# Kernel optimization log

Measured on AMD Instinct MI355X. Metric: run time of the kernel, lower is better.

## Reference

```python
import jax, jax.numpy as jnp
import numpy as np

T_, N_, DIN, D, HEADS, WW, E_, DPE = 8, 20000, 128, 128, 4, 4, 320000, 8
DH = D // HEADS
NEG = -1e30
EPS_GATE = 1e-6


def setup_inputs() -> dict:
    key = jax.random.key(0)
    ks = jax.random.split(key, 10)
    return {
        "H_tilde": jax.random.normal(ks[0], (T_, N_, DIN), jnp.float32),
        "S": jax.random.uniform(ks[1], (T_, N_), jnp.float32),
        "Wq": jax.random.normal(ks[2], (D, DIN), jnp.float32) * 0.05,
        "Wkh": jax.random.normal(ks[3], (D, DIN), jnp.float32) * 0.05,
        "Wkpe": jax.random.normal(ks[4], (D, DPE), jnp.float32) * 0.05,
        "Wv": jax.random.normal(ks[5], (D, DIN), jnp.float32) * 0.05,
        "pe_table": jax.random.normal(ks[6], (WW + 1, DPE), jnp.float32),
        "rel_bias": jax.random.normal(ks[7], (WW + 1,), jnp.float32),
        "src": jax.random.randint(ks[8], (E_,), 0, N_),
        "dst": jax.random.randint(ks[9], (E_,), 0, N_),
    }


def reference(H_tilde, S, Wq, Wkh, Wkpe, Wv, pe_table, rel_bias, src, dst):
    T, N, _ = H_tilde.shape
    H, dh, W = HEADS, DH, WW
    scale = dh ** -0.5
    dtype = H_tilde.dtype

    # Projections (torch Linear: x @ W.T). W_k over concat([H, pe]) splits additively.
    Q = (H_tilde @ Wq.T).reshape(T, N, H, dh)
    K0 = (H_tilde @ Wkh.T).reshape(T, N, H, dh)
    V = (H_tilde @ Wv.T).reshape(T, N, H, dh)
    pe_k = (pe_table @ Wkpe.T).reshape(W + 1, H, dh)
    gate = jnp.log(jnp.clip(S, 0.0, 1.0) + EPS_GATE)  # (T, N)

    # Pad W zero-steps in front so a length-(W+1) slice at t covers t-W..t.
    pad = lambda x: jnp.concatenate([jnp.zeros((W,) + x.shape[1:], x.dtype), x], axis=0)
    Kp, Vp, gp = pad(K0), pad(V), pad(gate)

    def step(_, tq):
        t, Qt = tq  # Qt: (N, H, dh)
        Kwin = jax.lax.dynamic_slice_in_dim(Kp, t, W + 1, 0)[::-1]  # (W+1,N,H,dh), dt=0..W
        Vwin = jax.lax.dynamic_slice_in_dim(Vp, t, W + 1, 0)[::-1]
        gwin = jax.lax.dynamic_slice_in_dim(gp, t, W + 1, 0)[::-1]  # (W+1, N)
        Qd = Qt[dst]  # (E, H, dh)

        scores = []
        for dt in range(W + 1):
            Ks = Kwin[dt][src] + pe_k[dt][None]  # (E, H, dh)
            s = (jnp.einsum('ehc,ehc->eh', Qd, Ks) * scale
                 + rel_bias[dt] + gwin[dt][src][:, None])
            scores.append(jnp.where(dt <= t, s, NEG))  # mask dt > t (W_eff = min(W, t))
        sc = jnp.stack(scores)  # (W+1, E, H)

        # Segment softmax over incoming edges of each dst node, jointly over dt.
        mx = jax.ops.segment_max(sc.transpose(1, 0, 2), dst, num_segments=N)  # (N,W+1,H)
        mx = mx.max(axis=1)  # (N, H)
        valid = (jnp.arange(W + 1) <= t)[:, None, None]
        ex = jnp.where(valid, jnp.exp(sc - mx[dst][None]), 0.0)  # (W+1, E, H)

        denom = jax.ops.segment_sum(ex.sum(axis=0), dst, num_segments=N)  # (N, H)
        numer = jnp.zeros((N, H, dh), dtype)
        for dt in range(W + 1):
            contrib = ex[dt][:, :, None] * Vwin[dt][src]  # (E, H, dh)
            numer = numer + jax.ops.segment_sum(contrib, dst, num_segments=N)

        msg = numer / jnp.maximum(denom, 1e-12)[:, :, None]  # (N, H, dh)
        return None, msg.reshape(N, H * dh)

    _, M_out = jax.lax.scan(step, None, (jnp.arange(T), Q))
    return M_out  # (T, N, d)
```

## Files before the change

kernel.cpp:

```cpp
#include <hip/hip_runtime.h>

typedef unsigned short u16;
typedef unsigned int u32;
typedef __attribute__((ext_vector_type(8))) __bf16 bf16x8;
typedef __attribute__((ext_vector_type(4))) float f32x4;
typedef __attribute__((ext_vector_type(4))) _Float16 f16x4;
typedef __attribute__((ext_vector_type(2))) unsigned u32x2;

constexpr int TT = 8, NN = 20000, DD = 128, EE = 320000;
constexpr int MAXDEG = 64;
constexpr float SCL = 0.17677669529663687f;
constexpr int VBLK2 = 544;

__device__ __forceinline__ u16 f2bf(float f) {
  return __builtin_bit_cast(u16, (__bf16)f);
}
__device__ __forceinline__ u16 f2h(float f) {
  return __builtin_bit_cast(u16, (_Float16)f);
}
__device__ __forceinline__ float blo(u32 u) { return __uint_as_float(u << 16); }
__device__ __forceinline__ float bhi(u32 u) { return __uint_as_float(u & 0xffff0000u); }

__device__ __forceinline__ bf16x8 cvt8(float4 f0, float4 f1) {
  bf16x8 r;
  r[0] = (__bf16)f0.x; r[1] = (__bf16)f0.y; r[2] = (__bf16)f0.z; r[3] = (__bf16)f0.w;
  r[4] = (__bf16)f1.x; r[5] = (__bf16)f1.y; r[6] = (__bf16)f1.z; r[7] = (__bf16)f1.w;
  return r;
}

__global__ void k_init(const float* __restrict__ pe_table, const float* __restrict__ Wkpe,
                       const float* __restrict__ Wq, const float* __restrict__ Wkh,
                       const float* __restrict__ Wv, const float* __restrict__ S,
                       float* __restrict__ pek, int* __restrict__ cnt,
                       u16* __restrict__ Wb, float* __restrict__ SgT) {
  int i = blockIdx.x * 256 + threadIdx.x;
  if (i < NN) cnt[i] = 0;
  if (i < 5 * DD) {
    int dt = i >> 7, j = i & 127;
    float s = 0.f;
    for (int p = 0; p < 8; ++p) s += pe_table[dt * 8 + p] * Wkpe[j * 8 + p];
    pek[i] = s;
  }
  if (i < 3 * DD * DD) {
    int y = i / (DD * DD), idx = i % (DD * DD);
    const float* W = (y == 0) ? Wq : (y == 1) ? Wkh : Wv;
    Wb[i] = f2bf(W[idx]);
  }
  if (i < TT * NN) {
    SgT[i] = fminf(fmaxf(S[i], 0.f), 1.f) + 1e-6f;
  }
}

__global__ void k_build(const int* __restrict__ src, const int* __restrict__ dst,
                        int* __restrict__ cnt, int* __restrict__ eslot) {
  int i = blockIdx.x * 256 + threadIdx.x;
  if (i < EE) {
    int d = dst[i];
    int p = atomicAdd(&cnt[d], 1);
    if (p < MAXDEG) eslot[d * MAXDEG + p] = src[i];
  }
}

__global__ __launch_bounds__(256) void k_proj6(
    const float* __restrict__ Hm, const u16* __restrict__ Wb,
    u16* __restrict__ Qb, u16* __restrict__ Kb, u16* __restrict__ Vb) {
  int tid = threadIdx.x;
  int lane = tid & 63, wv = tid >> 6;
  int wr = wv >> 1, wc = wv & 1;
  int l15 = lane & 15, lq = lane >> 4;
  size_t m0 = (size_t)blockIdx.x * 128;

  bf16x8 a[4][4];
#pragma unroll
  for (int ks = 0; ks < 4; ++ks) {
    int col0 = ks * 32 + lq * 8;
#pragma unroll
    for (int i = 0; i < 4; ++i) {
      const float* gp = Hm + (m0 + wr * 64 + i * 16 + l15) * DD + col0;
      a[ks][i] = cvt8(*(const float4*)gp, *(const float4*)(gp + 4));
    }
  }

  for (int y = 0; y < 3; ++y) {
    u16* Out = (y == 0) ? Qb : (y == 1) ? Kb : Vb;
    const bool asF16 = (y == 2);
    const float postm = (y == 0) ? SCL : 1.f;
    const u16* Wy = Wb + y * DD * DD;

    f32x4 acc[4][4];
    for (int i = 0; i < 4; ++i)
      for (int j = 0; j < 4; ++j) acc[i][j] = (f32x4){0.f, 0.f, 0.f, 0.f};

    for (int ks = 0; ks < 4; ++ks) {
      int col0 = ks * 32 + lq * 8;
      bf16x8 b[4];
#pragma unroll
      for (int j = 0; j < 4; ++j)
        b[j] = *(const bf16x8*)(Wy + (wc * 64 + j * 16 + l15) * DD + col0);
#pragma unroll
      for (int i = 0; i < 4; ++i)
#pragma unroll
        for (int j = 0; j < 4; ++j)
          acc[i][j] = __builtin_amdgcn_mfma_f32_16x16x32_bf16(a[ks][i], b[j], acc[i][j], 0, 0, 0);
    }

#pragma unroll
    for (int i = 0; i < 4; ++i)
#pragma unroll
      for (int j = 0; j < 4; ++j)
#pragma unroll
        for (int g = 0; g < 4; ++g) {
          size_t row = m0 + wr * 64 + i * 16 + lq * 4 + g;
          int col = wc * 64 + j * 16 + l15;
          float v = acc[i][j][g] * postm;
          Out[row * DD + col] = asF16 ? f2h(v) : f2bf(v);
        }
  }
}

__global__ __launch_bounds__(256, 8) void k_agg11(
    const u16* __restrict__ Qb, const u16* __restrict__ Kb, const u16* __restrict__ Vb,
    const float* __restrict__ SgT, const float* __restrict__ pek,
    const float* __restrict__ relb,
    const int* __restrict__ cnt, const int* __restrict__ eslot,
    float* __restrict__ outp) {
  __shared__ int srcB[MAXDEG];
  __shared__ float gateS[TT][MAXDEG];
  __shared__ float eW[4][TT][16];
  __shared__ u16 VldsS[4][VBLK2];
  int tid = threadIdx.x;
  const int h = tid >> 6, lane = tid & 63;
  const int n = blockIdx.x;

  int deg = min(cnt[n], MAXDEG);
  if (tid < MAXDEG) {
    int s = (tid < deg) ? eslot[n * MAXDEG + tid] : 0;
    srcB[tid] = s * DD;
  }
  for (int i = tid; i < TT * MAXDEG; i += 256) {
    int tp = i >> 6, e = i & 63;
    float g = 0.f;
    if (e < deg) g = SgT[(size_t)tp * NN + eslot[n * MAXDEG + e]];
    gateS[tp][e] = g;
  }

  const int t16 = lane & 15, qo = lane >> 4, qo4 = qo * 4;
  const int h32 = h * 32;

  uint4 qb;
  {
    bool qok = t16 < 8;
    const u16* Qp = Qb + ((size_t)(t16 & 7) * NN + n) * DD + h32 + qo * 8;
    qb = qok ? *(const uint4*)(Qp) : make_uint4(0u, 0u, 0u, 0u);
  }

  {
    ((float*)&eW[h][0][0])[lane] = -1e30f;
    ((float*)&eW[h][0][0])[lane + 64] = -1e30f;
    float qf0 = blo(qb.x), qf1 = bhi(qb.x), qf2 = blo(qb.y), qf3 = bhi(qb.y);
    float qf4 = blo(qb.z), qf5 = bhi(qb.z), qf6 = blo(qb.w), qf7 = bhi(qb.w);
#pragma unroll
    for (int d = 0; d < 5; ++d) {
      const float* pp = pek + d * DD + h32 + qo * 8;
      float4 p0 = *(const float4*)pp;
      float4 p1 = *(const float4*)(pp + 4);
      float s = qf0 * p0.x + qf1 * p0.y + qf2 * p0.z + qf3 * p0.w
              + qf4 * p1.x + qf5 * p1.y + qf6 * p1.z + qf7 * p1.w;
      s += __shfl_xor(s, 16);
      s += __shfl_xor(s, 32);
      int tp = t16 - d;
      if (qo == 0 && t16 < 8 && tp >= 0) eW[h][tp][t16] = s + relb[d];
    }
  }
  __syncthreads();

  f32x4 num0 = (f32x4){0.f, 0.f, 0.f, 0.f};
  f32x4 num1 = (f32x4){0.f, 0.f, 0.f, 0.f};
  float dd = 0.f;

  if (deg > 0) {
    const int degm1 = deg - 1;
    const int nch = (deg + 15) >> 4;
    const int cmax = nch << 4;
    const int nj = nch * 8;

    const int vkey = lane >> 2, vcb = lane & 3;
    u16* vbuf = &VldsS[h][0];
    unsigned trbase = (unsigned)(uintptr_t)vbuf + lane * 8;
    unsigned woff = (unsigned)((vcb >> 1) * VBLK2 + (vkey >> 2) * 128 +
                               (vkey & 3) * 32 + (vcb & 1) * 16);
    const float* eWt = &eW[h][0][t16];

    auto loadK = [&](int tp, int c16) -> uint4 {
      return *(const uint4*)(Kb + (size_t)tp * (NN * DD)
                             + (size_t)srcB[min(c16 + t16, degm1)] + h32 + qo * 8);
    };
    auto loadV = [&](int tp, int c16) -> uint4 {
      return *(const uint4*)(Vb + (size_t)tp * (NN * DD)
                             + (size_t)srcB[min(c16 + vkey, degm1)] + h32 + vcb * 8);
    };
    auto loadG = [&](int tp, int c16) -> f32x4 {
      return *(const f32x4*)&gateS[tp][c16 + qo4];
    };
    auto writeV = [&](uint4 f) { *(uint4*)((char*)vbuf + woff) = f; };
    auto compute = [&](uint4 ka, f32x4 g4, int tp) {
      float Lf = eWt[tp * 16];

      f32x4 z = (f32x4){0.f, 0.f, 0.f, 0.f};
      f32x4 sc = __builtin_amdgcn_mfma_f32_16x16x32_bf16(
          __builtin_bit_cast(bf16x8, ka), __builtin_bit_cast(bf16x8, qb), z, 0, 0, 0);

      float w0 = __expf(sc[0] + Lf) * g4[0];
      float w1 = __expf(sc[1] + Lf) * g4[1];
      float w2 = __expf(sc[2] + Lf) * g4[2];
      float w3 = __expf(sc[3] + Lf) * g4[3];
      dd += w0 + w1 + w2 + w3;
      f16x4 wf;
      wf[0] = (_Float16)w0; wf[1] = (_Float16)w1;
      wf[2] = (_Float16)w2; wf[3] = (_Float16)w3;

      __builtin_amdgcn_sched_barrier(0);
      u32x2 vr0, vr1;
      asm volatile("ds_read_b64_tr_b16 %0, %1" : "=v"(vr0) : "v"(trbase));
      asm volatile("ds_read_b64_tr_b16 %0, %1 offset:544" : "=v"(vr1) : "v"(trbase));
      asm volatile("s_waitcnt lgkmcnt(0)");
      __builtin_amdgcn_sched_barrier(0);
      num0 = __builtin_amdgcn_mfma_f32_16x16x16f16(
          wf, __builtin_bit_cast(f16x4, vr0), num0, 0, 0, 0);
      num1 = __builtin_amdgcn_mfma_f32_16x16x16f16(
          wf, __builtin_bit_cast(f16x4, vr1), num1, 0, 0, 0);
    };

    uint4 kA = loadK(0, 0);
    f32x4 gA = loadG(0, 0);
    writeV(loadV(0, 0));
    int tpj = 0;
    int tpn = 0, cn = 16;
    if (cn >= cmax) { cn = 0; tpn = 1; }

    for (int j = 0; j < nj; ++j) {
      bool more = (j + 1) < nj;
      uint4 kB = make_uint4(0u, 0u, 0u, 0u), vB = make_uint4(0u, 0u, 0u, 0u);
      f32x4 gB = (f32x4){0.f, 0.f, 0.f, 0.f};
      if (more) {
        kB = loadK(tpn, cn);
        vB = loadV(tpn, cn);
        gB = loadG(tpn, cn);
      }
      compute(kA, gA, tpj);
      __builtin_amdgcn_sched_barrier(0);
      if (more) writeV(vB);
      kA = kB;
      gA = gB;
      tpj = tpn;
      cn += 16;
      if (cn >= cmax) { cn = 0; ++tpn; }
    }
  }

  float Dh = dd;
  Dh += __shfl_xor(Dh, 16);
  Dh += __shfl_xor(Dh, 32);
#pragma unroll
  for (int r = 0; r < 4; ++r) {
    int t = qo4 + r;
    float Dt = __shfl(Dh, t);
    if (t < 8) {
      float inv = 1.f / fmaxf(Dt, 1e-12f);
      float* op = outp + ((size_t)t * NN + n) * DD + h32;
      op[t16] = num0[r] * inv;
      op[16 + t16] = num1[r] * inv;
    }
  }
}

extern "C" void kernel_launch(void* const* d_in, const int* in_sizes, int n_in,
                              void* d_out, int out_size, void* d_ws, size_t ws_size,
                              hipStream_t stream) {
  const float* Hm = (const float*)d_in[0];
  const float* S = (const float*)d_in[1];
  const float* Wq = (const float*)d_in[2];
  const float* Wkh = (const float*)d_in[3];
  const float* Wkpe = (const float*)d_in[4];
  const float* Wv = (const float*)d_in[5];
  const float* pe_table = (const float*)d_in[6];
  const float* relb = (const float*)d_in[7];
  const int* src = (const int*)d_in[8];
  const int* dst = (const int*)d_in[9];
  float* out = (float*)d_out;

  auto aup = [](size_t x) { return (x + 255) & ~(size_t)255; };
  char* base = (char*)d_ws;
  size_t off = 0;
  u16* Qb = (u16*)(base + off); off = aup(off + (size_t)TT * NN * DD * 2);
  u16* Kb = (u16*)(base + off); off = aup(off + (size_t)TT * NN * DD * 2);
  u16* Vb = (u16*)(base + off); off = aup(off + (size_t)TT * NN * DD * 2);
  float* pek = (float*)(base + off); off = aup(off + (size_t)5 * DD * 4);
  float* SgT = (float*)(base + off); off = aup(off + (size_t)TT * NN * 4);
  int* cnt = (int*)(base + off); off = aup(off + (size_t)NN * 4);
  int* eslot = (int*)(base + off); off = aup(off + (size_t)NN * MAXDEG * 4);
  u16* Wb = (u16*)(base + off); off = aup(off + (size_t)3 * DD * DD * 2);
  (void)ws_size; (void)in_sizes; (void)n_in; (void)out_size;

  k_init<<<(TT * NN + 255) / 256, 256, 0, stream>>>(pe_table, Wkpe, Wq, Wkh, Wv, S,
                                                    pek, cnt, Wb, SgT);
  k_build<<<(EE + 255) / 256, 256, 0, stream>>>(src, dst, cnt, eslot);
  k_proj6<<<1250, 256, 0, stream>>>(Hm, Wb, Qb, Kb, Vb);
  k_agg11<<<NN, 256, 0, stream>>>(Qb, Kb, Vb, SgT, pek, relb, cnt, eslot, out);
}
```

Before: 302.1 us.

## Store K/V head-major and map each aggregation wave to its own node

The projection kernel now writes K and V in a head-major layout (head, t, node, 32), while Q keeps its original layout. In the aggregation kernel each block handles one head for four nodes, one wave per node. Each wave loads its own source list and gate values, so the block-wide barrier is no longer needed and each K/V gather reads from a compact per-head slab. In exchange, the edge slots and gate values for a node are now fetched once per head instead of once per node, and the index arithmetic for the scattered stores gets more complex.

```diff
diff --git a/kernel.cpp b/kernel.cpp
--- a/kernel.cpp
+++ b/kernel.cpp
@@ -61,7 +61,7 @@
   }
 }
 
-__global__ __launch_bounds__(256) void k_proj6(
+__global__ __launch_bounds__(256) void k_proj7(
     const float* __restrict__ Hm, const u16* __restrict__ Wb,
     u16* __restrict__ Qb, u16* __restrict__ Kb, u16* __restrict__ Vb) {
   int tid = threadIdx.x;
@@ -110,42 +110,46 @@
       for (int j = 0; j < 4; ++j)
 #pragma unroll
         for (int g = 0; g < 4; ++g) {
-          size_t row = m0 + wr * 64 + i * 16 + lq * 4 + g;
+          u32 row = (u32)(m0 + wr * 64 + i * 16 + lq * 4 + g);
           int col = wc * 64 + j * 16 + l15;
           float v = acc[i][j][g] * postm;
-          Out[row * DD + col] = asF16 ? f2h(v) : f2bf(v);
+          if (y == 0) {
+            Out[(size_t)row * DD + col] = f2bf(v);
+          } else {
+            u32 t = row / (u32)NN;
+            u32 nn_ = row - t * (u32)NN;
+            int hh = col >> 5, cc = col & 31;
+            Out[(((size_t)hh * TT + t) * NN + nn_) * 32 + cc]
+                = asF16 ? f2h(v) : f2bf(v);
+          }
         }
   }
 }
 
-__global__ __launch_bounds__(256, 8) void k_agg11(
+__global__ __launch_bounds__(256, 8) void k_agg12(
     const u16* __restrict__ Qb, const u16* __restrict__ Kb, const u16* __restrict__ Vb,
     const float* __restrict__ SgT, const float* __restrict__ pek,
     const float* __restrict__ relb,
     const int* __restrict__ cnt, const int* __restrict__ eslot,
     float* __restrict__ outp) {
-  __shared__ int srcB[MAXDEG];
-  __shared__ float gateS[TT][MAXDEG];
-  __shared__ float eW[4][TT][16];
+  __shared__ int srcW[4][MAXDEG];
+  __shared__ float gateW[4][TT][MAXDEG];
+  __shared__ float eWW[4][TT][16];
   __shared__ u16 VldsS[4][VBLK2];
   int tid = threadIdx.x;
-  const int h = tid >> 6, lane = tid & 63;
-  const int n = blockIdx.x;
+  const int wv = tid >> 6, lane = tid & 63;
+  const int h = blockIdx.x & 3;
+  const int n = (blockIdx.x >> 2) * 4 + wv;
+  const int h32 = h * 32;
 
   int deg = min(cnt[n], MAXDEG);
-  if (tid < MAXDEG) {
-    int s = (tid < deg) ? eslot[n * MAXDEG + tid] : 0;
-    srcB[tid] = s * DD;
-  }
-  for (int i = tid; i < TT * MAXDEG; i += 256) {
-    int tp = i >> 6, e = i & 63;
-    float g = 0.f;
-    if (e < deg) g = SgT[(size_t)tp * NN + eslot[n * MAXDEG + e]];
-    gateS[tp][e] = g;
-  }
+  int s_e = (lane < deg) ? eslot[n * MAXDEG + lane] : 0;
+  srcW[wv][lane] = s_e * 32;
+#pragma unroll
+  for (int tp = 0; tp < TT; ++tp)
+    gateW[wv][tp][lane] = (lane < deg) ? SgT[(size_t)tp * NN + s_e] : 0.f;
 
   const int t16 = lane & 15, qo = lane >> 4, qo4 = qo * 4;
-  const int h32 = h * 32;
 
   uint4 qb;
   {
@@ -155,8 +159,8 @@
   }
 
   {
-    ((float*)&eW[h][0][0])[lane] = -1e30f;
-    ((float*)&eW[h][0][0])[lane + 64] = -1e30f;
+    ((float*)&eWW[wv][0][0])[lane] = -1e30f;
+    ((float*)&eWW[wv][0][0])[lane + 64] = -1e30f;
     float qf0 = blo(qb.x), qf1 = bhi(qb.x), qf2 = blo(qb.y), qf3 = bhi(qb.y);
     float qf4 = blo(qb.z), qf5 = bhi(qb.z), qf6 = blo(qb.w), qf7 = bhi(qb.w);
 #pragma unroll
@@ -169,10 +173,9 @@
       s += __shfl_xor(s, 16);
       s += __shfl_xor(s, 32);
       int tp = t16 - d;
-      if (qo == 0 && t16 < 8 && tp >= 0) eW[h][tp][t16] = s + relb[d];
-    }
-  }
-  __syncthreads();
+      if (qo == 0 && t16 < 8 && tp >= 0) eWW[wv][tp][t16] = s + relb[d];
+    }
+  }
 
   f32x4 num0 = (f32x4){0.f, 0.f, 0.f, 0.f};
   f32x4 num1 = (f32x4){0.f, 0.f, 0.f, 0.f};
@@ -185,22 +188,24 @@
     const int nj = nch * 8;
 
     const int vkey = lane >> 2, vcb = lane & 3;
-    u16* vbuf = &VldsS[h][0];
+    u16* vbuf = &VldsS[wv][0];
     unsigned trbase = (unsigned)(uintptr_t)vbuf + lane * 8;
     unsigned woff = (unsigned)((vcb >> 1) * VBLK2 + (vkey >> 2) * 128 +
                                (vkey & 3) * 32 + (vcb & 1) * 16);
-    const float* eWt = &eW[h][0][t16];
+    const float* eWt = &eWW[wv][0][t16];
+    const u16* Kh = Kb + (size_t)h * TT * NN * 32;
+    const u16* Vh = Vb + (size_t)h * TT * NN * 32;
 
     auto loadK = [&](int tp, int c16) -> uint4 {
-      return *(const uint4*)(Kb + (size_t)tp * (NN * DD)
-                             + (size_t)srcB[min(c16 + t16, degm1)] + h32 + qo * 8);
+      return *(const uint4*)(Kh + (size_t)tp * (NN * 32)
+                             + (size_t)srcW[wv][min(c16 + t16, degm1)] + qo * 8);
     };
     auto loadV = [&](int tp, int c16) -> uint4 {
-      return *(const uint4*)(Vb + (size_t)tp * (NN * DD)
-                             + (size_t)srcB[min(c16 + vkey, degm1)] + h32 + vcb * 8);
+      return *(const uint4*)(Vh + (size_t)tp * (NN * 32)
+                             + (size_t)srcW[wv][min(c16 + vkey, degm1)] + vcb * 8);
     };
     auto loadG = [&](int tp, int c16) -> f32x4 {
-      return *(const f32x4*)&gateS[tp][c16 + qo4];
+      return *(const f32x4*)&gateW[wv][tp][c16 + qo4];
     };
     auto writeV = [&](uint4 f) { *(uint4*)((char*)vbuf + woff) = f; };
     auto compute = [&](uint4 ka, f32x4 g4, int tp) {
@@ -305,6 +310,6 @@
   k_init<<<(TT * NN + 255) / 256, 256, 0, stream>>>(pe_table, Wkpe, Wq, Wkh, Wv, S,
                                                     pek, cnt, Wb, SgT);
   k_build<<<(EE + 255) / 256, 256, 0, stream>>>(src, dst, cnt, eslot);
-  k_proj6<<<1250, 256, 0, stream>>>(Hm, Wb, Qb, Kb, Vb);
-  k_agg11<<<NN, 256, 0, stream>>>(Qb, Kb, Vb, SgT, pek, relb, cnt, eslot, out);
-}
+  k_proj7<<<1250, 256, 0, stream>>>(Hm, Wb, Qb, Kb, Vb);
+  k_agg12<<<NN, 256, 0, stream>>>(Qb, Kb, Vb, SgT, pek, relb, cnt, eslot, out);
+}
```

Result: slower. 438.7 us (+45.2%).
